# Optimization experiments

Hardware: AMD Instinct MI355X
Metric: run time of the kernel (lower is better)

## Reference

```python
import jax, jax.numpy as jnp
import numpy as np

B, T, M, D, H = 32, 256, 16, 128, 128

def _hard_sigmoid(x):
    # Keras hard_sigmoid: clip(0.2*x + 0.5, 0, 1)
    return jnp.clip(0.2 * x + 0.5, 0.0, 1.0)

def setup_inputs() -> dict:
    key = jax.random.key(0)
    ks = jax.random.split(key, 16)
    s = 0.05  # small init scale, roughly glorot-ish for these dims
    inp = {"x": jax.random.normal(ks[0], (B, T, M, D), jnp.float32)}
    inp["W_a"] = jax.random.normal(ks[1], (D + H, H), jnp.float32) * s
    inp["b_a"] = jnp.zeros((H,), jnp.float32)
    for i, n in enumerate("ifco"):
        inp[f"W_{n}"] = jax.random.normal(ks[2 + 3 * i], (D, H), jnp.float32) * s
        inp[f"U_{n}"] = jax.random.normal(ks[3 + 3 * i], (H, H), jnp.float32) * s
        inp[f"b_{n}"] = jnp.ones((H,), jnp.float32) if n == "f" else jnp.zeros((H,), jnp.float32)
    return inp

def reference(x, W_a, b_a, W_i, U_i, b_i, W_f, U_f, b_f, W_c, U_c, b_c, W_o, U_o, b_o):
    b, t, m, d = x.shape
    h_dim = W_i.shape[1]

    def step(carry, x_t):  # x_t: (B, M, D)
        h, c = carry  # each (B, H)
        hb = jnp.broadcast_to(h[:, None, :], (b, m, h_dim))
        con = jnp.concatenate([x_t, hb], axis=-1)          # (B, M, D+H)
        scores = (con @ W_a + b_a).sum(axis=-1)            # (B, M), linear activation
        sm = jax.nn.softmax(scores, axis=-1)               # (B, M)
        new_x = jnp.einsum('bm,bmd->bd', sm, x_t)          # attention-pooled input
        i_g = _hard_sigmoid(new_x @ W_i + b_i + h @ U_i)
        f_g = _hard_sigmoid(new_x @ W_f + b_f + h @ U_f)
        c_new = f_g * c + i_g * jnp.tanh(new_x @ W_c + b_c + h @ U_c)
        o_g = _hard_sigmoid(new_x @ W_o + b_o + h @ U_o)
        h_new = o_g * jnp.tanh(c_new)
        return (h_new, c_new), None

    h0 = jnp.zeros((b, h_dim), x.dtype)
    c0 = jnp.zeros((b, h_dim), x.dtype)
    (h_last, _), _ = jax.lax.scan(step, (h0, c0), jnp.swapaxes(x, 0, 1))
    return h_last  # return_sequences=False -> last output (B, H)
```

## Files before the change

kernel.cpp:

```cpp
#include <hip/hip_runtime.h>
#include <hip/hip_bf16.h>
#include <hip/hip_fp16.h>

#define BB 32
#define TT 256
#define MM 16
#define DD 128
#define HH 128

typedef unsigned int uint;
typedef unsigned short ushort;

typedef _Float16 f16;
typedef _Float16 f16x8 __attribute__((ext_vector_type(8)));
typedef float f32x4 __attribute__((ext_vector_type(4)));

__device__ __forceinline__ float bl16(uint u){ return __uint_as_float(u << 16); }
__device__ __forceinline__ float bh16(uint u){ return __uint_as_float(u & 0xffff0000u); }

__device__ __forceinline__ float hsig(float x){
  return __builtin_amdgcn_fmed3f(fmaf(x, 0.2f, 0.5f), 0.0f, 1.0f);
}
__device__ __forceinline__ float tanh_f(float x){
  return 1.0f - 2.0f / (__expf(2.0f * x) + 1.0f);
}

__device__ __forceinline__ uint packh2(float a, float b){
  __half2 hv = __floats2half2_rn(a, b);
  union{__half2 h; uint x;} cv; cv.h = hv; return cv.x;
}

__device__ __forceinline__ float qsum4(float v){
  float t1 = __int_as_float(__builtin_amdgcn_mov_dpp(__float_as_int(v), 0xB1, 0xf, 0xf, true));
  v += t1;
  float t2 = __int_as_float(__builtin_amdgcn_mov_dpp(__float_as_int(v), 0x4E, 0xf, 0xf, true));
  return v + t2;
}

__global__ __launch_bounds__(256) void k_prep(
  const void* __restrict__ xraw, const void* __restrict__ Wa,
  const void* __restrict__ U0, const void* __restrict__ U1,
  const void* __restrict__ U2, const void* __restrict__ U3,
  const void* __restrict__ W0, const void* __restrict__ W1,
  const void* __restrict__ W2, const void* __restrict__ W3,
  int* __restrict__ flag, float* __restrict__ vx,
  uint4* __restrict__ Uw, uint4* __restrict__ Ww)
{
  __shared__ int cnt[256];
  __shared__ int smode;
  int tid = threadIdx.x;
  int bid = blockIdx.x;

  {
    const ushort* u = (const ushort*)xraw;
    int c = 0;
    #pragma unroll
    for (int j = 0; j < 8; ++j){
      ushort v = u[2 * (tid * 8 + j)];
      float f = __uint_as_float(((uint)v) << 16);
      if (f == f && fabsf(f) < 64.f && fabsf(f) > 1e-12f) ++c;
    }
    cnt[tid] = c;
    __syncthreads();
    if (tid == 0){
      int s = 0;
      for (int i = 0; i < 256; ++i) s += cnt[i];
      smode = (s > 1024) ? 1 : 0;
    }
    __syncthreads();
  }
  int mode = smode;

  if (bid < 64){
    int idx = (bid & 31) * 256 + tid;
    int f = idx >> 6, lane = idx & 63;
    int g = f >> 5, kc = (f >> 3) & 3, cb = f & 7;
    int k0 = kc * 32 + (lane >> 4) * 8;
    int c  = cb * 16 + (lane & 15);
    const void* Ms[4];
    if (bid < 32){ Ms[0] = U0; Ms[1] = U1; Ms[2] = U2; Ms[3] = U3; }
    else         { Ms[0] = W0; Ms[1] = W1; Ms[2] = W2; Ms[3] = W3; }
    float v[8];
    if (mode){
      const ushort* U = (const ushort*)Ms[g];
      #pragma unroll
      for (int e = 0; e < 8; ++e)
        v[e] = __uint_as_float(((uint)U[(size_t)(k0 + e) * HH + c]) << 16);
    } else {
      const float* U = (const float*)Ms[g];
      #pragma unroll
      for (int e = 0; e < 8; ++e)
        v[e] = U[(size_t)(k0 + e) * HH + c];
    }
    uint4 o;
    o.x = packh2(v[0], v[1]); o.y = packh2(v[2], v[3]);
    o.z = packh2(v[4], v[5]); o.w = packh2(v[6], v[7]);
    ((bid < 32) ? Uw : Ww)[idx] = o;
  } else {
    if (tid == 0) *flag = mode;
    if (tid < 128){
      int d = tid;
      float s = 0.f;
      if (mode){
        const uint4* row = (const uint4*)((const ushort*)Wa + d * HH);
        #pragma unroll
        for (int q = 0; q < 16; ++q){
          uint4 v = row[q];
          s += bl16(v.x) + bh16(v.x) + bl16(v.y) + bh16(v.y)
             + bl16(v.z) + bh16(v.z) + bl16(v.w) + bh16(v.w);
        }
      } else {
        const float4* row = (const float4*)((const float*)Wa + d * HH);
        #pragma unroll
        for (int q = 0; q < 32; ++q){
          float4 v = row[q];
          s += v.x + v.y + v.z + v.w;
        }
      }
      vx[d] = s;
    }
  }
}

__global__ __launch_bounds__(256) void k_pool(const void* __restrict__ xraw,
                                              const int* __restrict__ flag,
                                              const float* __restrict__ vx,
                                              __half* __restrict__ newx){
  __shared__ float xs[2][MM][DD];
  __shared__ float sc[2][MM];
  int mode = *flag;
  int tid = threadIdx.x;
  int half = tid >> 7, t2 = tid & 127;
  int bt = blockIdx.x * 2 + half;
  int b = bt >> 8, t = bt & 255;

  float* xdst = &xs[half][0][0];
  if (mode){
    const float* vxp = vx + (t2 & 15) * 8;
    float4 vra = *(const float4*)vxp;
    float4 vrb = *(const float4*)(vxp + 4);
    const uint4* s = (const uint4*)((const ushort*)xraw + (size_t)bt * 2048);
    float sq[2];
    #pragma unroll
    for (int q = 0; q < 2; ++q){
      int ch = t2 + 128 * q;
      uint4 v = s[ch];
      float* d = &xdst[ch * 8];
      float e0 = bl16(v.x), e1 = bh16(v.x), e2 = bl16(v.y), e3 = bh16(v.y);
      float e4 = bl16(v.z), e5 = bh16(v.z), e6 = bl16(v.w), e7 = bh16(v.w);
      d[0] = e0; d[1] = e1; d[2] = e2; d[3] = e3;
      d[4] = e4; d[5] = e5; d[6] = e6; d[7] = e7;
      float p = e0 * vra.x;
      p = fmaf(e1, vra.y, p); p = fmaf(e2, vra.z, p); p = fmaf(e3, vra.w, p);
      p = fmaf(e4, vrb.x, p); p = fmaf(e5, vrb.y, p); p = fmaf(e6, vrb.z, p);
      p = fmaf(e7, vrb.w, p);
      sq[q] = p;
    }
    #pragma unroll
    for (int q = 0; q < 2; ++q){
      float v = qsum4(sq[q]);
      v += __shfl_xor(v, 4, 16);
      v += __shfl_xor(v, 8, 16);
      sq[q] = v;
    }
    if ((t2 & 15) == 0){
      sc[half][t2 >> 4]       = sq[0];
      sc[half][(t2 >> 4) + 8] = sq[1];
    }
  } else {
    float4 vra = *(const float4*)(vx + (t2 & 31) * 4);
    const float4* s = (const float4*)((const float*)xraw + (size_t)bt * 2048);
    float sq[4];
    #pragma unroll
    for (int q = 0; q < 4; ++q){
      int ch = t2 + 128 * q;
      float4 v = s[ch];
      *(float4*)&xdst[ch * 4] = v;
      float p = v.x * vra.x;
      p = fmaf(v.y, vra.y, p); p = fmaf(v.z, vra.z, p); p = fmaf(v.w, vra.w, p);
      sq[q] = p;
    }
    #pragma unroll
    for (int q = 0; q < 4; ++q){
      float v = qsum4(sq[q]);
      v += __shfl_xor(v, 4, 32);
      v += __shfl_xor(v, 8, 32);
      v += __shfl_xor(v, 16, 32);
      sq[q] = v;
    }
    if ((t2 & 31) == 0){
      int mb = t2 >> 5;
      sc[half][mb]      = sq[0];
      sc[half][mb + 4]  = sq[1];
      sc[half][mb + 8]  = sq[2];
      sc[half][mb + 12] = sq[3];
    }
  }
  __syncthreads();

  float mx = sc[half][0];
  #pragma unroll
  for (int m2 = 1; m2 < MM; ++m2) mx = fmaxf(mx, sc[half][m2]);
  float wgt[MM]; float den = 0.f;
  #pragma unroll
  for (int m2 = 0; m2 < MM; ++m2){ wgt[m2] = __expf(sc[half][m2] - mx); den += wgt[m2]; }
  float inv = 1.0f / den;

  float acc = 0.f;
  #pragma unroll
  for (int m2 = 0; m2 < MM; ++m2)
    acc = fmaf(wgt[m2], xs[half][m2][t2], acc);
  newx[((size_t)t * BB + b) * DD + t2] = __float2half(acc * inv);
}

__global__ __launch_bounds__(256) void k_xproj(const __half* __restrict__ nx,
  const uint4* __restrict__ Ww,
  const void* __restrict__ b0_, const void* __restrict__ b1_,
  const void* __restrict__ b2_, const void* __restrict__ b3_,
  const int* __restrict__ flag, float* __restrict__ Xp)
{
  __shared__ __align__(16) char As[32768];
  int tid = threadIdx.x;
  int r0 = blockIdx.x * 128;
  int G  = blockIdx.y;
  int lane = tid & 63, w = tid >> 6;
  int l16 = lane & 15, lq = lane >> 4;

  {
    const uint4* src = (const uint4*)(nx + (size_t)r0 * DD);
    uint4* dst = (uint4*)As;
    #pragma unroll
    for (int i = 0; i < 8; ++i){
      int gid = i * 256 + tid;
      int r = gid >> 4, c16 = gid & 15;
      dst[r * 16 + (c16 ^ (r & 15))] = src[gid];
    }
  }

  int mode = *flag;
  const void* bb = (G == 0) ? b0_ : (G == 1) ? b1_ : (G == 2) ? b2_ : b3_;
  float bias[8];
  #pragma unroll
  for (int cb = 0; cb < 8; ++cb){
    int col = cb * 16 + l16;
    bias[cb] = mode ? __uint_as_float(((uint)((const ushort*)bb)[col]) << 16)
                    : ((const float*)bb)[col];
  }
  __syncthreads();

  int rb = w * 32;
  f32x4 acc[2][8];
  #pragma unroll
  for (int mt = 0; mt < 2; ++mt)
    #pragma unroll
    for (int cb = 0; cb < 8; ++cb)
      acc[mt][cb] = (f32x4){bias[cb], bias[cb], bias[cb], bias[cb]};

  #pragma unroll
  for (int kc = 0; kc < 4; ++kc){
    f16x8 a[2];
    #pragma unroll
    for (int mt = 0; mt < 2; ++mt){
      int r = rb + mt * 16 + l16;
      int g16 = (kc * 4 + lq) ^ (r & 15);
      a[mt] = *(const f16x8*)(As + r * 256 + g16 * 16);
    }
    #pragma unroll
    for (int cb = 0; cb < 8; ++cb){
      union{uint4 u; f16x8 h;} bv;
      bv.u = Ww[((size_t)((G * 4 + kc) * 8 + cb)) * 64 + lane];
      acc[0][cb] = __builtin_amdgcn_mfma_f32_16x16x32_f16(a[0], bv.h, acc[0][cb], 0, 0, 0);
      acc[1][cb] = __builtin_amdgcn_mfma_f32_16x16x32_f16(a[1], bv.h, acc[1][cb], 0, 0, 0);
    }
  }

  #pragma unroll
  for (int mt = 0; mt < 2; ++mt)
    #pragma unroll
    for (int cb = 0; cb < 8; ++cb)
      #pragma unroll
      for (int reg = 0; reg < 4; ++reg){
        size_t r = (size_t)(r0 + rb + mt * 16 + lq * 4 + reg);
        Xp[r * 512 + G * HH + cb * 16 + l16] = acc[mt][cb][reg];
      }
}

__global__ __attribute__((amdgpu_waves_per_eu(2, 2))) __launch_bounds__(512)
void k_rec(const float* __restrict__ Xp, const uint4* __restrict__ Uw,
           float* __restrict__ out)
{
  __shared__ __align__(16) __half hlds[2][HH];
  int tid  = threadIdx.x;
  int b    = blockIdx.x;
  int w    = tid >> 6;
  int lane = tid & 63;
  int l16  = lane & 15;

  f16x8 Ub[16];
  #pragma unroll
  for (int g = 0; g < 4; ++g)
    #pragma unroll
    for (int kc = 0; kc < 4; ++kc){
      uint4 v = Uw[((g * 4 + kc) * 8 + w) * 64 + lane];
      union{uint4 u; f16x8 h;} cv; cv.u = v;
      Ub[g * 4 + kc] = cv.h;
    }

  const float* xcol = Xp + (size_t)b * 512 + w * 16 + l16;
  float xpA[4], xpB[4];
  #pragma unroll
  for (int g = 0; g < 4; ++g) xpA[g] = xcol[g * 128];
  #pragma unroll
  for (int g = 0; g < 4; ++g) xpB[g] = xcol[(size_t)(BB * 512) + g * 128];

  if (tid < 64) ((uint*)&hlds[0][0])[tid] = 0;
  float cst = 0.f, vh = 0.f;
  const int lo = (lane >> 4) * 16;
  __syncthreads();

#define STEP(T, XP) do{                                                        \
    const char* hb = (const char*)&hlds[(T) & 1][0];                           \
    f16x8 a0 = *(const f16x8*)(hb +   0 + lo);                                 \
    f16x8 a1 = *(const f16x8*)(hb +  64 + lo);                                 \
    f16x8 a2 = *(const f16x8*)(hb + 128 + lo);                                 \
    f16x8 a3 = *(const f16x8*)(hb + 192 + lo);                                 \
    f32x4 c0, c1, c2, c3, d0, d1, d2, d3;                                      \
    c0[0] = XP[0]; c1[0] = XP[1]; c2[0] = XP[2]; c3[0] = XP[3];                \
    d0[0] = 0.f;   d1[0] = 0.f;   d2[0] = 0.f;   d3[0] = 0.f;                  \
    c0 = __builtin_amdgcn_mfma_f32_16x16x32_f16(a0, Ub[ 0], c0, 0, 0, 0);      \
    c1 = __builtin_amdgcn_mfma_f32_16x16x32_f16(a0, Ub[ 4], c1, 0, 0, 0);      \
    c2 = __builtin_amdgcn_mfma_f32_16x16x32_f16(a0, Ub[ 8], c2, 0, 0, 0);      \
    c3 = __builtin_amdgcn_mfma_f32_16x16x32_f16(a0, Ub[12], c3, 0, 0, 0);      \
    d0 = __builtin_amdgcn_mfma_f32_16x16x32_f16(a2, Ub[ 2], d0, 0, 0, 0);      \
    d1 = __builtin_amdgcn_mfma_f32_16x16x32_f16(a2, Ub[ 6], d1, 0, 0, 0);      \
    d2 = __builtin_amdgcn_mfma_f32_16x16x32_f16(a2, Ub[10], d2, 0, 0, 0);      \
    d3 = __builtin_amdgcn_mfma_f32_16x16x32_f16(a2, Ub[14], d3, 0, 0, 0);      \
    c0 = __builtin_amdgcn_mfma_f32_16x16x32_f16(a1, Ub[ 1], c0, 0, 0, 0);      \
    c1 = __builtin_amdgcn_mfma_f32_16x16x32_f16(a1, Ub[ 5], c1, 0, 0, 0);      \
    c2 = __builtin_amdgcn_mfma_f32_16x16x32_f16(a1, Ub[ 9], c2, 0, 0, 0);      \
    c3 = __builtin_amdgcn_mfma_f32_16x16x32_f16(a1, Ub[13], c3, 0, 0, 0);      \
    d0 = __builtin_amdgcn_mfma_f32_16x16x32_f16(a3, Ub[ 3], d0, 0, 0, 0);      \
    d1 = __builtin_amdgcn_mfma_f32_16x16x32_f16(a3, Ub[ 7], d1, 0, 0, 0);      \
    d2 = __builtin_amdgcn_mfma_f32_16x16x32_f16(a3, Ub[11], d2, 0, 0, 0);      \
    d3 = __builtin_amdgcn_mfma_f32_16x16x32_f16(a3, Ub[15], d3, 0, 0, 0);      \
    float p0 = c0[0] + d0[0];                                                  \
    float p1 = c1[0] + d1[0];                                                  \
    float p2 = c2[0] + d2[0];                                                  \
    float p3 = c3[0] + d3[0];                                                  \
    float ig = hsig(p0), fg = hsig(p1), og = hsig(p3);                         \
    float gg = tanh_f(p2);                                                     \
    cst = fmaf(fg, cst, ig * gg);                                              \
    vh  = og * tanh_f(cst);                                                    \
    if (lane < 16) hlds[((T) + 1) & 1][w * 16 + lane] = __float2half(vh);      \
    {                                                                          \
      int tp = (T) + 2; if (tp > TT - 1) tp = TT - 1;                          \
      const float* xs = xcol + ((size_t)tp << 14);                             \
      _Pragma("unroll")                                                        \
      for (int g = 0; g < 4; ++g) XP[g] = xs[g * 128];                         \
    }                                                                          \
    asm volatile("s_waitcnt lgkmcnt(0)" ::: "memory");                         \
    __builtin_amdgcn_s_barrier();                                              \
    asm volatile("" ::: "memory");                                             \
  }while(0)

  for (int t = 0; t < TT; t += 2){
    STEP(t,     xpA);
    STEP(t + 1, xpB);
  }
#undef STEP

  if (lane < 16) out[b * HH + w * 16 + lane] = vh;
}

extern "C" void kernel_launch(void* const* d_in, const int* in_sizes, int n_in,
                              void* d_out, int out_size, void* d_ws, size_t ws_size,
                              hipStream_t stream) {
  (void)in_sizes; (void)n_in; (void)out_size; (void)ws_size;

  char* ws = (char*)d_ws;
  int* flag = (int*)ws;
  float* vx = (float*)(ws + 16);
  uint4* Uw = (uint4*)(ws + 1024);
  uint4* Ww = (uint4*)(ws + 1024 + 131072);
  __half* newx = (__half*)(ws + 1024 + 2 * 131072);
  float* Xp = (float*)(ws + 1024 + 2 * 131072 + (size_t)2 * 1024 * 1024);

  k_prep<<<65, 256, 0, stream>>>(d_in[0], d_in[1],
      d_in[4], d_in[7], d_in[10], d_in[13],
      d_in[3], d_in[6], d_in[9],  d_in[12],
      flag, vx, Uw, Ww);
  k_pool<<<BB * TT / 2, 256, 0, stream>>>(d_in[0], flag, vx, newx);
  dim3 g2(64, 4);
  k_xproj<<<g2, 256, 0, stream>>>(newx, Ww,
      d_in[5], d_in[8], d_in[11], d_in[14],
      flag, Xp);
  k_rec<<<BB, 512, 0, stream>>>(Xp, Uw, (float*)d_out);
}
```

Measured before the change: 251.7 us.

## Fuse prep, pooling, projection and recurrence into one cooperative kernel

Replaces the four separate launches (weight repack, attention pooling, input projection, recurrence) with a single cooperative kernel that separates phases with grid-wide syncs, falling back to the old launches if the cooperative launch fails. This aims to remove launch gaps and kernel-boundary overhead between stages. The trade-off is that the recurrence still runs on only 32 of 256 blocks, the pooling phase is restricted to 256 resident blocks, and grid syncs add their own cost.

Measured after the change: 345.2 us. 37.1% more time.

```diff
diff --git a/kernel.cpp b/kernel.cpp
--- a/kernel.cpp
+++ b/kernel.cpp
@@ -1,12 +1,16 @@
 #include <hip/hip_runtime.h>
+#include <hip/hip_cooperative_groups.h>
 #include <hip/hip_bf16.h>
 #include <hip/hip_fp16.h>
+
+namespace cg = cooperative_groups;
 
 #define BB 32
 #define TT 256
 #define MM 16
 #define DD 128
 #define HH 128
+#define GRID 256
 
 typedef unsigned int uint;
 typedef unsigned short ushort;
@@ -24,17 +28,326 @@
 __device__ __forceinline__ float tanh_f(float x){
   return 1.0f - 2.0f / (__expf(2.0f * x) + 1.0f);
 }
-
 __device__ __forceinline__ uint packh2(float a, float b){
   __half2 hv = __floats2half2_rn(a, b);
   union{__half2 h; uint x;} cv; cv.h = hv; return cv.x;
 }
-
 __device__ __forceinline__ float qsum4(float v){
   float t1 = __int_as_float(__builtin_amdgcn_mov_dpp(__float_as_int(v), 0xB1, 0xf, 0xf, true));
   v += t1;
   float t2 = __int_as_float(__builtin_amdgcn_mov_dpp(__float_as_int(v), 0x4E, 0xf, 0xf, true));
   return v + t2;
+}
+
+__global__ __attribute__((amdgpu_waves_per_eu(2, 2))) __launch_bounds__(512)
+void k_fused(const void* __restrict__ xraw, const void* __restrict__ Wa,
+  const void* __restrict__ U0, const void* __restrict__ U1,
+  const void* __restrict__ U2, const void* __restrict__ U3,
+  const void* __restrict__ W0, const void* __restrict__ W1,
+  const void* __restrict__ W2, const void* __restrict__ W3,
+  const void* __restrict__ b0_, const void* __restrict__ b1_,
+  const void* __restrict__ b2_, const void* __restrict__ b3_,
+  uint4* __restrict__ Uw, uint4* __restrict__ Ww,
+  __half* __restrict__ newx, float* __restrict__ Xp,
+  float* __restrict__ out)
+{
+  __shared__ float xs[4][MM][DD];
+  __shared__ float sc4[4][MM];
+  __shared__ __align__(16) float part4[512];
+  __shared__ __align__(16) float vxs[DD];
+  __shared__ int cnt[256];
+  __shared__ int smode;
+  __shared__ __align__(16) __half hlds[2][HH];
+
+  cg::grid_group grid = cg::this_grid();
+  int tid = threadIdx.x;
+  int bid = blockIdx.x;
+  int lane = tid & 63;
+  int wv = tid >> 6;
+
+  if (tid < 256){
+    const ushort* u = (const ushort*)xraw;
+    int c = 0;
+    #pragma unroll
+    for (int j = 0; j < 8; ++j){
+      ushort v = u[2 * (tid * 8 + j)];
+      float f = __uint_as_float(((uint)v) << 16);
+      if (f == f && fabsf(f) < 64.f && fabsf(f) > 1e-12f) ++c;
+    }
+    cnt[tid] = c;
+  }
+  __syncthreads();
+  if (tid == 0){
+    int s = 0;
+    for (int i = 0; i < 256; ++i) s += cnt[i];
+    smode = (s > 1024) ? 1 : 0;
+  }
+  __syncthreads();
+  int mode = smode;
+
+  {
+    int gtid = bid * 512 + tid;
+    if (gtid < 16384){
+      int half = gtid >> 13;
+      int idx = gtid & 8191;
+      int f = idx >> 6, pl = idx & 63;
+      int g = f >> 5, kc = (f >> 3) & 3, cb = f & 7;
+      int k0 = kc * 32 + (pl >> 4) * 8;
+      int c  = cb * 16 + (pl & 15);
+      const void* Ms[8] = {U0, U1, U2, U3, W0, W1, W2, W3};
+      const void* M = Ms[half * 4 + g];
+      float v[8];
+      if (mode){
+        const ushort* U = (const ushort*)M;
+        #pragma unroll
+        for (int e = 0; e < 8; ++e)
+          v[e] = __uint_as_float(((uint)U[(size_t)(k0 + e) * HH + c]) << 16);
+      } else {
+        const float* U = (const float*)M;
+        #pragma unroll
+        for (int e = 0; e < 8; ++e)
+          v[e] = U[(size_t)(k0 + e) * HH + c];
+      }
+      uint4 o;
+      o.x = packh2(v[0], v[1]); o.y = packh2(v[2], v[3]);
+      o.z = packh2(v[4], v[5]); o.w = packh2(v[6], v[7]);
+      (half ? Ww : Uw)[idx] = o;
+    }
+  }
+
+  {
+    int d = tid >> 2, q = tid & 3;
+    float s = 0.f;
+    if (mode){
+      const uint4* row = (const uint4*)((const ushort*)Wa + d * HH + q * 32);
+      #pragma unroll
+      for (int qq = 0; qq < 4; ++qq){
+        uint4 v = row[qq];
+        s += bl16(v.x) + bh16(v.x) + bl16(v.y) + bh16(v.y)
+           + bl16(v.z) + bh16(v.z) + bl16(v.w) + bh16(v.w);
+      }
+    } else {
+      const float4* row = (const float4*)((const float*)Wa + d * HH + q * 32);
+      #pragma unroll
+      for (int qq = 0; qq < 8; ++qq){
+        float4 v = row[qq];
+        s += v.x + v.y + v.z + v.w;
+      }
+    }
+    part4[tid] = s;
+  }
+  __syncthreads();
+  if (tid < 128)
+    vxs[tid] = part4[4 * tid] + part4[4 * tid + 1] + part4[4 * tid + 2] + part4[4 * tid + 3];
+
+  for (int pass = 0; pass < 8; ++pass){
+    int q4 = tid >> 7, t2 = tid & 127;
+    int bt = pass * 1024 + bid * 4 + q4;
+    int b = bt >> 8, t = bt & 255;
+    float* xdst = &xs[q4][0][0];
+    __syncthreads();
+    if (mode){
+      const float* vxp = &vxs[(t2 & 15) * 8];
+      float4 vra = *(const float4*)vxp;
+      float4 vrb = *(const float4*)(vxp + 4);
+      const uint4* s = (const uint4*)((const ushort*)xraw + (size_t)bt * 2048);
+      float sq[2];
+      #pragma unroll
+      for (int q = 0; q < 2; ++q){
+        int ch = t2 + 128 * q;
+        uint4 v = s[ch];
+        float* d = &xdst[ch * 8];
+        float e0 = bl16(v.x), e1 = bh16(v.x), e2 = bl16(v.y), e3 = bh16(v.y);
+        float e4 = bl16(v.z), e5 = bh16(v.z), e6 = bl16(v.w), e7 = bh16(v.w);
+        d[0] = e0; d[1] = e1; d[2] = e2; d[3] = e3;
+        d[4] = e4; d[5] = e5; d[6] = e6; d[7] = e7;
+        float p = e0 * vra.x;
+        p = fmaf(e1, vra.y, p); p = fmaf(e2, vra.z, p); p = fmaf(e3, vra.w, p);
+        p = fmaf(e4, vrb.x, p); p = fmaf(e5, vrb.y, p); p = fmaf(e6, vrb.z, p);
+        p = fmaf(e7, vrb.w, p);
+        sq[q] = p;
+      }
+      #pragma unroll
+      for (int q = 0; q < 2; ++q){
+        float v = qsum4(sq[q]);
+        v += __shfl_xor(v, 4, 16);
+        v += __shfl_xor(v, 8, 16);
+        sq[q] = v;
+      }
+      if ((t2 & 15) == 0){
+        sc4[q4][t2 >> 4]       = sq[0];
+        sc4[q4][(t2 >> 4) + 8] = sq[1];
+      }
+    } else {
+      float4 vra = *(const float4*)&vxs[(t2 & 31) * 4];
+      const float4* s = (const float4*)((const float*)xraw + (size_t)bt * 2048);
+      float sq[4];
+      #pragma unroll
+      for (int q = 0; q < 4; ++q){
+        int ch = t2 + 128 * q;
+        float4 v = s[ch];
+        *(float4*)&xdst[ch * 4] = v;
+        float p = v.x * vra.x;
+        p = fmaf(v.y, vra.y, p); p = fmaf(v.z, vra.z, p); p = fmaf(v.w, vra.w, p);
+        sq[q] = p;
+      }
+      #pragma unroll
+      for (int q = 0; q < 4; ++q){
+        float v = qsum4(sq[q]);
+        v += __shfl_xor(v, 4, 32);
+        v += __shfl_xor(v, 8, 32);
+        v += __shfl_xor(v, 16, 32);
+        sq[q] = v;
+      }
+      if ((t2 & 31) == 0){
+        int mb = t2 >> 5;
+        sc4[q4][mb]      = sq[0];
+        sc4[q4][mb + 4]  = sq[1];
+        sc4[q4][mb + 8]  = sq[2];
+        sc4[q4][mb + 12] = sq[3];
+      }
+    }
+    __syncthreads();
+
+    float mx = sc4[q4][0];
+    #pragma unroll
+    for (int m2 = 1; m2 < MM; ++m2) mx = fmaxf(mx, sc4[q4][m2]);
+    float wgt[MM]; float den = 0.f;
+    #pragma unroll
+    for (int m2 = 0; m2 < MM; ++m2){ wgt[m2] = __expf(sc4[q4][m2] - mx); den += wgt[m2]; }
+    float inv = 1.0f / den;
+
+    float acc = 0.f;
+    #pragma unroll
+    for (int m2 = 0; m2 < MM; ++m2)
+      acc = fmaf(wgt[m2], xs[q4][m2][t2], acc);
+    newx[((size_t)t * BB + b) * DD + t2] = __float2half(acc * inv);
+  }
+
+  grid.sync();
+
+  {
+    int wg = bid * 8 + wv;
+    int rc = wg >> 2, G = wg & 3;
+    int r0 = rc * 16;
+    int l16 = lane & 15, lq = lane >> 4;
+
+    const void* bb = (G == 0) ? b0_ : (G == 1) ? b1_ : (G == 2) ? b2_ : b3_;
+    float bias[8];
+    #pragma unroll
+    for (int cb = 0; cb < 8; ++cb){
+      int col = cb * 16 + l16;
+      bias[cb] = mode ? __uint_as_float(((uint)((const ushort*)bb)[col]) << 16)
+                      : ((const float*)bb)[col];
+    }
+
+    f16x8 a[4];
+    #pragma unroll
+    for (int kc = 0; kc < 4; ++kc)
+      a[kc] = *(const f16x8*)(newx + (size_t)(r0 + l16) * DD + kc * 32 + lq * 8);
+
+    f32x4 acc[8];
+    #pragma unroll
+    for (int cb = 0; cb < 8; ++cb)
+      acc[cb] = (f32x4){bias[cb], bias[cb], bias[cb], bias[cb]};
+
+    #pragma unroll
+    for (int kc = 0; kc < 4; ++kc)
+      #pragma unroll
+      for (int cb = 0; cb < 8; ++cb){
+        union{uint4 u; f16x8 h;} bv;
+        bv.u = Ww[((size_t)((G * 4 + kc) * 8 + cb)) * 64 + lane];
+        acc[cb] = __builtin_amdgcn_mfma_f32_16x16x32_f16(a[kc], bv.h, acc[cb], 0, 0, 0);
+      }
+
+    #pragma unroll
+    for (int cb = 0; cb < 8; ++cb)
+      #pragma unroll
+      for (int reg = 0; reg < 4; ++reg)
+        Xp[(size_t)(r0 + lq * 4 + reg) * 512 + G * HH + cb * 16 + l16] = acc[cb][reg];
+  }
+
+  grid.sync();
+
+  if (bid < BB){
+    int b = bid;
+    int l16 = lane & 15;
+
+    f16x8 Ub[16];
+    #pragma unroll
+    for (int g = 0; g < 4; ++g)
+      #pragma unroll
+      for (int kc = 0; kc < 4; ++kc){
+        uint4 v = Uw[((g * 4 + kc) * 8 + wv) * 64 + lane];
+        union{uint4 u; f16x8 h;} cv; cv.u = v;
+        Ub[g * 4 + kc] = cv.h;
+      }
+
+    const float* xcol = Xp + (size_t)b * 512 + wv * 16 + l16;
+    float xpA[4], xpB[4];
+    #pragma unroll
+    for (int g = 0; g < 4; ++g) xpA[g] = xcol[g * 128];
+    #pragma unroll
+    for (int g = 0; g < 4; ++g) xpB[g] = xcol[(size_t)(BB * 512) + g * 128];
+
+    if (tid < 64) ((uint*)&hlds[0][0])[tid] = 0;
+    float cst = 0.f, vh = 0.f;
+    const int lo = (lane >> 4) * 16;
+    __syncthreads();
+
+#define STEP(T, XP) do{                                                        \
+    const char* hb = (const char*)&hlds[(T) & 1][0];                           \
+    f16x8 a0 = *(const f16x8*)(hb +   0 + lo);                                 \
+    f16x8 a1 = *(const f16x8*)(hb +  64 + lo);                                 \
+    f16x8 a2 = *(const f16x8*)(hb + 128 + lo);                                 \
+    f16x8 a3 = *(const f16x8*)(hb + 192 + lo);                                 \
+    f32x4 c0, c1, c2, c3, d0, d1, d2, d3;                                      \
+    c0[0] = XP[0]; c1[0] = XP[1]; c2[0] = XP[2]; c3[0] = XP[3];                \
+    d0[0] = 0.f;   d1[0] = 0.f;   d2[0] = 0.f;   d3[0] = 0.f;                  \
+    c0 = __builtin_amdgcn_mfma_f32_16x16x32_f16(a0, Ub[ 0], c0, 0, 0, 0);      \
+    c1 = __builtin_amdgcn_mfma_f32_16x16x32_f16(a0, Ub[ 4], c1, 0, 0, 0);      \
+    c2 = __builtin_amdgcn_mfma_f32_16x16x32_f16(a0, Ub[ 8], c2, 0, 0, 0);      \
+    c3 = __builtin_amdgcn_mfma_f32_16x16x32_f16(a0, Ub[12], c3, 0, 0, 0);      \
+    d0 = __builtin_amdgcn_mfma_f32_16x16x32_f16(a2, Ub[ 2], d0, 0, 0, 0);      \
+    d1 = __builtin_amdgcn_mfma_f32_16x16x32_f16(a2, Ub[ 6], d1, 0, 0, 0);      \
+    d2 = __builtin_amdgcn_mfma_f32_16x16x32_f16(a2, Ub[10], d2, 0, 0, 0);      \
+    d3 = __builtin_amdgcn_mfma_f32_16x16x32_f16(a2, Ub[14], d3, 0, 0, 0);      \
+    c0 = __builtin_amdgcn_mfma_f32_16x16x32_f16(a1, Ub[ 1], c0, 0, 0, 0);      \
+    c1 = __builtin_amdgcn_mfma_f32_16x16x32_f16(a1, Ub[ 5], c1, 0, 0, 0);      \
+    c2 = __builtin_amdgcn_mfma_f32_16x16x32_f16(a1, Ub[ 9], c2, 0, 0, 0);      \
+    c3 = __builtin_amdgcn_mfma_f32_16x16x32_f16(a1, Ub[13], c3, 0, 0, 0);      \
+    d0 = __builtin_amdgcn_mfma_f32_16x16x32_f16(a3, Ub[ 3], d0, 0, 0, 0);      \
+    d1 = __builtin_amdgcn_mfma_f32_16x16x32_f16(a3, Ub[ 7], d1, 0, 0, 0);      \
+    d2 = __builtin_amdgcn_mfma_f32_16x16x32_f16(a3, Ub[11], d2, 0, 0, 0);      \
+    d3 = __builtin_amdgcn_mfma_f32_16x16x32_f16(a3, Ub[15], d3, 0, 0, 0);      \
+    float p0 = c0[0] + d0[0];                                                  \
+    float p1 = c1[0] + d1[0];                                                  \
+    float p2 = c2[0] + d2[0];                                                  \
+    float p3 = c3[0] + d3[0];                                                  \
+    float ig = hsig(p0), fg = hsig(p1), og = hsig(p3);                         \
+    float gg = tanh_f(p2);                                                     \
+    cst = fmaf(fg, cst, ig * gg);                                              \
+    vh  = og * tanh_f(cst);                                                    \
+    if (lane < 16) hlds[((T) + 1) & 1][wv * 16 + lane] = __float2half(vh);     \
+    {                                                                          \
+      int tp = (T) + 2; if (tp > TT - 1) tp = TT - 1;                          \
+      const float* xsrc = xcol + ((size_t)tp << 14);                           \
+      _Pragma("unroll")                                                        \
+      for (int g = 0; g < 4; ++g) XP[g] = xsrc[g * 128];                       \
+    }                                                                          \
+    asm volatile("s_waitcnt lgkmcnt(0)" ::: "memory");                         \
+    __builtin_amdgcn_s_barrier();                                              \
+    asm volatile("" ::: "memory");                                             \
+  }while(0)
+
+    for (int t = 0; t < TT; t += 2){
+      STEP(t,     xpA);
+      STEP(t + 1, xpB);
+    }
+#undef STEP
+
+    if (lane < 16) out[b * HH + wv * 16 + lane] = vh;
+  }
 }
 
 __global__ __launch_bounds__(256) void k_prep(
@@ -50,7 +363,6 @@
   __shared__ int smode;
   int tid = threadIdx.x;
   int bid = blockIdx.x;
-
   {
     const ushort* u = (const ushort*)xraw;
     int c = 0;
@@ -354,9 +666,9 @@
     if (lane < 16) hlds[((T) + 1) & 1][w * 16 + lane] = __float2half(vh);      \
     {                                                                          \
       int tp = (T) + 2; if (tp > TT - 1) tp = TT - 1;                          \
-      const float* xs = xcol + ((size_t)tp << 14);                             \
+      const float* xsrc = xcol + ((size_t)tp << 14);                           \
       _Pragma("unroll")                                                        \
-      for (int g = 0; g < 4; ++g) XP[g] = xs[g * 128];                         \
+      for (int g = 0; g < 4; ++g) XP[g] = xsrc[g * 128];                       \
     }                                                                          \
     asm volatile("s_waitcnt lgkmcnt(0)" ::: "memory");                         \
     __builtin_amdgcn_s_barrier();                                              \
@@ -385,14 +697,37 @@
   __half* newx = (__half*)(ws + 1024 + 2 * 131072);
   float* Xp = (float*)(ws + 1024 + 2 * 131072 + (size_t)2 * 1024 * 1024);
 
-  k_prep<<<65, 256, 0, stream>>>(d_in[0], d_in[1],
-      d_in[4], d_in[7], d_in[10], d_in[13],
-      d_in[3], d_in[6], d_in[9],  d_in[12],
-      flag, vx, Uw, Ww);
-  k_pool<<<BB * TT / 2, 256, 0, stream>>>(d_in[0], flag, vx, newx);
-  dim3 g2(64, 4);
-  k_xproj<<<g2, 256, 0, stream>>>(newx, Ww,
-      d_in[5], d_in[8], d_in[11], d_in[14],
-      flag, Xp);
-  k_rec<<<BB, 512, 0, stream>>>(Xp, Uw, (float*)d_out);
-}
+  void* p_x  = (void*)d_in[0];  void* p_wa = (void*)d_in[1];
+  void* p_u0 = (void*)d_in[4];  void* p_u1 = (void*)d_in[7];
+  void* p_u2 = (void*)d_in[10]; void* p_u3 = (void*)d_in[13];
+  void* p_w0 = (void*)d_in[3];  void* p_w1 = (void*)d_in[6];
+  void* p_w2 = (void*)d_in[9];  void* p_w3 = (void*)d_in[12];
+  void* p_b0 = (void*)d_in[5];  void* p_b1 = (void*)d_in[8];
+  void* p_b2 = (void*)d_in[11]; void* p_b3 = (void*)d_in[14];
+  void* p_out = d_out;
+
+  void* kargs[] = {
+    &p_x, &p_wa,
+    &p_u0, &p_u1, &p_u2, &p_u3,
+    &p_w0, &p_w1, &p_w2, &p_w3,
+    &p_b0, &p_b1, &p_b2, &p_b3,
+    &Uw, &Ww, &newx, &Xp, &p_out
+  };
+
+  hipError_t err = hipLaunchCooperativeKernel(
+      reinterpret_cast<const void*>(&k_fused),
+      dim3(GRID), dim3(512), kargs, 0, stream);
+
+  if (err != hipSuccess){
+    k_prep<<<65, 256, 0, stream>>>(d_in[0], d_in[1],
+        d_in[4], d_in[7], d_in[10], d_in[13],
+        d_in[3], d_in[6], d_in[9],  d_in[12],
+        flag, vx, Uw, Ww);
+    k_pool<<<BB * TT / 2, 256, 0, stream>>>(d_in[0], flag, vx, newx);
+    dim3 g2(64, 4);
+    k_xproj<<<g2, 256, 0, stream>>>(newx, Ww,
+        d_in[5], d_in[8], d_in[11], d_in[14],
+        flag, Xp);
+    k_rec<<<BB, 512, 0, stream>>>(Xp, Uw, (float*)d_out);
+  }
+}
```

## Fuse prep with pooling and fold input projection into recurrent kernel

Applied to the files above, without the earlier changes.

Merges the weight-prep and attention-pooling kernels into one launch: each pooling block recomputes the row sums of W_a in shared memory and redetects the input mode, so no flag or vx buffer is needed. The input-projection GEMM moves into the recurrent kernel, where each batch block computes its own Xp slice before the time loop. This removes two kernel launches and the associated dependencies. In exchange, the projection runs on only 32 blocks with strided loads, which may serialize work that was previously spread across many blocks.

After: 292.8 us. 16.3% more time.

```diff
diff --git a/kernel.cpp b/kernel.cpp
--- a/kernel.cpp
+++ b/kernel.cpp
@@ -24,12 +24,10 @@
 __device__ __forceinline__ float tanh_f(float x){
   return 1.0f - 2.0f / (__expf(2.0f * x) + 1.0f);
 }
-
 __device__ __forceinline__ uint packh2(float a, float b){
   __half2 hv = __floats2half2_rn(a, b);
   union{__half2 h; uint x;} cv; cv.h = hv; return cv.x;
 }
-
 __device__ __forceinline__ float qsum4(float v){
   float t1 = __int_as_float(__builtin_amdgcn_mov_dpp(__float_as_int(v), 0xB1, 0xf, 0xf, true));
   v += t1;
@@ -37,16 +35,20 @@
   return v + t2;
 }
 
-__global__ __launch_bounds__(256) void k_prep(
+
+__global__ __launch_bounds__(256) void k_prep_pool(
   const void* __restrict__ xraw, const void* __restrict__ Wa,
   const void* __restrict__ U0, const void* __restrict__ U1,
   const void* __restrict__ U2, const void* __restrict__ U3,
   const void* __restrict__ W0, const void* __restrict__ W1,
   const void* __restrict__ W2, const void* __restrict__ W3,
-  int* __restrict__ flag, float* __restrict__ vx,
-  uint4* __restrict__ Uw, uint4* __restrict__ Ww)
+  uint4* __restrict__ Uw, uint4* __restrict__ Ww,
+  __half* __restrict__ newx)
 {
-  __shared__ int cnt[256];
+  __shared__ float xs[2][MM][DD];
+  __shared__ float sc[2][MM];
+  __shared__ __align__(16) float vxs[DD];
+  __shared__ int wcnt[4];
   __shared__ int smode;
   int tid = threadIdx.x;
   int bid = blockIdx.x;
@@ -60,13 +62,11 @@
       float f = __uint_as_float(((uint)v) << 16);
       if (f == f && fabsf(f) < 64.f && fabsf(f) > 1e-12f) ++c;
     }
-    cnt[tid] = c;
+    #pragma unroll
+    for (int off = 1; off < 64; off <<= 1) c += __shfl_xor(c, off, 64);
+    if ((tid & 63) == 0) wcnt[tid >> 6] = c;
     __syncthreads();
-    if (tid == 0){
-      int s = 0;
-      for (int i = 0; i < 256; ++i) s += cnt[i];
-      smode = (s > 1024) ? 1 : 0;
-    }
+    if (tid == 0) smode = (wcnt[0] + wcnt[1] + wcnt[2] + wcnt[3] > 1024) ? 1 : 0;
     __syncthreads();
   }
   int mode = smode;
@@ -96,47 +96,40 @@
     o.x = packh2(v[0], v[1]); o.y = packh2(v[2], v[3]);
     o.z = packh2(v[4], v[5]); o.w = packh2(v[6], v[7]);
     ((bid < 32) ? Uw : Ww)[idx] = o;
-  } else {
-    if (tid == 0) *flag = mode;
-    if (tid < 128){
-      int d = tid;
-      float s = 0.f;
-      if (mode){
-        const uint4* row = (const uint4*)((const ushort*)Wa + d * HH);
-        #pragma unroll
-        for (int q = 0; q < 16; ++q){
-          uint4 v = row[q];
-          s += bl16(v.x) + bh16(v.x) + bl16(v.y) + bh16(v.y)
-             + bl16(v.z) + bh16(v.z) + bl16(v.w) + bh16(v.w);
-        }
-      } else {
-        const float4* row = (const float4*)((const float*)Wa + d * HH);
-        #pragma unroll
-        for (int q = 0; q < 32; ++q){
-          float4 v = row[q];
-          s += v.x + v.y + v.z + v.w;
-        }
-      }
-      vx[d] = s;
-    }
-  }
-}
-
-__global__ __launch_bounds__(256) void k_pool(const void* __restrict__ xraw,
-                                              const int* __restrict__ flag,
-                                              const float* __restrict__ vx,
-                                              __half* __restrict__ newx){
-  __shared__ float xs[2][MM][DD];
-  __shared__ float sc[2][MM];
-  int mode = *flag;
-  int tid = threadIdx.x;
+    return;
+  }
+
+  {
+    int d = tid >> 1, q = tid & 1;
+    float s = 0.f;
+    if (mode){
+      const uint4* row = (const uint4*)((const ushort*)Wa + d * HH + q * 64);
+      #pragma unroll
+      for (int qq = 0; qq < 8; ++qq){
+        uint4 v = row[qq];
+        s += bl16(v.x) + bh16(v.x) + bl16(v.y) + bh16(v.y)
+           + bl16(v.z) + bh16(v.z) + bl16(v.w) + bh16(v.w);
+      }
+    } else {
+      const float4* row = (const float4*)((const float*)Wa + d * HH + q * 64);
+      #pragma unroll
+      for (int qq = 0; qq < 16; ++qq){
+        float4 v = row[qq];
+        s += v.x + v.y + v.z + v.w;
+      }
+    }
+    s += __shfl_xor(s, 1, 64);
+    if (q == 0) vxs[d] = s;
+  }
+  __syncthreads();
+
   int half = tid >> 7, t2 = tid & 127;
-  int bt = blockIdx.x * 2 + half;
+  int bt = (bid - 64) * 2 + half;
   int b = bt >> 8, t = bt & 255;
 
   float* xdst = &xs[half][0][0];
   if (mode){
-    const float* vxp = vx + (t2 & 15) * 8;
+    const float* vxp = &vxs[(t2 & 15) * 8];
     float4 vra = *(const float4*)vxp;
     float4 vrb = *(const float4*)(vxp + 4);
     const uint4* s = (const uint4*)((const ushort*)xraw + (size_t)bt * 2048);
@@ -168,7 +161,7 @@
       sc[half][(t2 >> 4) + 8] = sq[1];
     }
   } else {
-    float4 vra = *(const float4*)(vx + (t2 & 31) * 4);
+    float4 vra = *(const float4*)&vxs[(t2 & 31) * 4];
     const float4* s = (const float4*)((const float*)xraw + (size_t)bt * 2048);
     float sq[4];
     #pragma unroll
@@ -213,100 +206,99 @@
   newx[((size_t)t * BB + b) * DD + t2] = __float2half(acc * inv);
 }
 
-__global__ __launch_bounds__(256) void k_xproj(const __half* __restrict__ nx,
-  const uint4* __restrict__ Ww,
-  const void* __restrict__ b0_, const void* __restrict__ b1_,
-  const void* __restrict__ b2_, const void* __restrict__ b3_,
-  const int* __restrict__ flag, float* __restrict__ Xp)
-{
-  __shared__ __align__(16) char As[32768];
-  int tid = threadIdx.x;
-  int r0 = blockIdx.x * 128;
-  int G  = blockIdx.y;
-  int lane = tid & 63, w = tid >> 6;
-  int l16 = lane & 15, lq = lane >> 4;
-
-  {
-    const uint4* src = (const uint4*)(nx + (size_t)r0 * DD);
-    uint4* dst = (uint4*)As;
-    #pragma unroll
-    for (int i = 0; i < 8; ++i){
-      int gid = i * 256 + tid;
-      int r = gid >> 4, c16 = gid & 15;
-      dst[r * 16 + (c16 ^ (r & 15))] = src[gid];
-    }
-  }
-
-  int mode = *flag;
-  const void* bb = (G == 0) ? b0_ : (G == 1) ? b1_ : (G == 2) ? b2_ : b3_;
-  float bias[8];
-  #pragma unroll
-  for (int cb = 0; cb < 8; ++cb){
-    int col = cb * 16 + l16;
-    bias[cb] = mode ? __uint_as_float(((uint)((const ushort*)bb)[col]) << 16)
-                    : ((const float*)bb)[col];
-  }
-  __syncthreads();
-
-  int rb = w * 32;
-  f32x4 acc[2][8];
-  #pragma unroll
-  for (int mt = 0; mt < 2; ++mt)
-    #pragma unroll
-    for (int cb = 0; cb < 8; ++cb)
-      acc[mt][cb] = (f32x4){bias[cb], bias[cb], bias[cb], bias[cb]};
-
-  #pragma unroll
-  for (int kc = 0; kc < 4; ++kc){
-    f16x8 a[2];
-    #pragma unroll
-    for (int mt = 0; mt < 2; ++mt){
-      int r = rb + mt * 16 + l16;
-      int g16 = (kc * 4 + lq) ^ (r & 15);
-      a[mt] = *(const f16x8*)(As + r * 256 + g16 * 16);
-    }
-    #pragma unroll
-    for (int cb = 0; cb < 8; ++cb){
-      union{uint4 u; f16x8 h;} bv;
-      bv.u = Ww[((size_t)((G * 4 + kc) * 8 + cb)) * 64 + lane];
-      acc[0][cb] = __builtin_amdgcn_mfma_f32_16x16x32_f16(a[0], bv.h, acc[0][cb], 0, 0, 0);
-      acc[1][cb] = __builtin_amdgcn_mfma_f32_16x16x32_f16(a[1], bv.h, acc[1][cb], 0, 0, 0);
-    }
-  }
-
-  #pragma unroll
-  for (int mt = 0; mt < 2; ++mt)
-    #pragma unroll
-    for (int cb = 0; cb < 8; ++cb)
-      #pragma unroll
-      for (int reg = 0; reg < 4; ++reg){
-        size_t r = (size_t)(r0 + rb + mt * 16 + lq * 4 + reg);
-        Xp[r * 512 + G * HH + cb * 16 + l16] = acc[mt][cb][reg];
-      }
-}
-
 __global__ __attribute__((amdgpu_waves_per_eu(2, 2))) __launch_bounds__(512)
-void k_rec(const float* __restrict__ Xp, const uint4* __restrict__ Uw,
-           float* __restrict__ out)
+void k_rec2(const void* __restrict__ xraw, const __half* __restrict__ newx,
+            const uint4* __restrict__ Uw, const uint4* __restrict__ Ww,
+            const void* __restrict__ b0_, const void* __restrict__ b1_,
+            const void* __restrict__ b2_, const void* __restrict__ b3_,
+            float* __restrict__ Xp, float* __restrict__ out)
 {
   __shared__ __align__(16) __half hlds[2][HH];
+  __shared__ int wcnt[8];
+  __shared__ int smode;
   int tid  = threadIdx.x;
   int b    = blockIdx.x;
-  int w    = tid >> 6;
+  int wv   = tid >> 6;
   int lane = tid & 63;
-  int l16  = lane & 15;
+  int l16  = lane & 15, lq = lane >> 4;
+
+  {
+    const ushort* u = (const ushort*)xraw;
+    int c = 0;
+    #pragma unroll
+    for (int j = 0; j < 4; ++j){
+      ushort v = u[2 * (tid * 4 + j)];
+      float f = __uint_as_float(((uint)v) << 16);
+      if (f == f && fabsf(f) < 64.f && fabsf(f) > 1e-12f) ++c;
+    }
+    #pragma unroll
+    for (int off = 1; off < 64; off <<= 1) c += __shfl_xor(c, off, 64);
+    if (lane == 0) wcnt[wv] = c;
+    __syncthreads();
+    if (tid == 0){
+      int s = 0;
+      #pragma unroll
+      for (int i = 0; i < 8; ++i) s += wcnt[i];
+      smode = (s > 1024) ? 1 : 0;
+    }
+    __syncthreads();
+  }
+  int mode = smode;
+
+  {
+    int tc0 = wv, tc1 = wv + 8;
+    for (int G = 0; G < 4; ++G){
+      const void* bb = (G == 0) ? b0_ : (G == 1) ? b1_ : (G == 2) ? b2_ : b3_;
+      float bias[8];
+      #pragma unroll
+      for (int cb = 0; cb < 8; ++cb){
+        int col = cb * 16 + l16;
+        bias[cb] = mode ? __uint_as_float(((uint)((const ushort*)bb)[col]) << 16)
+                        : ((const float*)bb)[col];
+      }
+      f32x4 acc0[8], acc1[8];
+      #pragma unroll
+      for (int cb = 0; cb < 8; ++cb){
+        acc0[cb] = (f32x4){bias[cb], bias[cb], bias[cb], bias[cb]};
+        acc1[cb] = (f32x4){bias[cb], bias[cb], bias[cb], bias[cb]};
+      }
+      #pragma unroll
+      for (int kc = 0; kc < 4; ++kc){
+        f16x8 a0 = *(const f16x8*)(newx + ((size_t)(tc0 * 16 + l16) * BB + b) * DD + kc * 32 + lq * 8);
+        f16x8 a1 = *(const f16x8*)(newx + ((size_t)(tc1 * 16 + l16) * BB + b) * DD + kc * 32 + lq * 8);
+        #pragma unroll
+        for (int cb = 0; cb < 8; ++cb){
+          union{uint4 u; f16x8 h;} bv;
+          bv.u = Ww[((size_t)((G * 4 + kc) * 8 + cb)) * 64 + lane];
+          acc0[cb] = __builtin_amdgcn_mfma_f32_16x16x32_f16(a0, bv.h, acc0[cb], 0, 0, 0);
+          acc1[cb] = __builtin_amdgcn_mfma_f32_16x16x32_f16(a1, bv.h, acc1[cb], 0, 0, 0);
+        }
+      }
+      #pragma unroll
+      for (int cb = 0; cb < 8; ++cb)
+        #pragma unroll
+        for (int reg = 0; reg < 4; ++reg){
+          int t0 = tc0 * 16 + lq * 4 + reg;
+          int t1 = tc1 * 16 + lq * 4 + reg;
+          Xp[((size_t)t0 * BB + b) * 512 + G * HH + cb * 16 + l16] = acc0[cb][reg];
+          Xp[((size_t)t1 * BB + b) * 512 + G * HH + cb * 16 + l16] = acc1[cb][reg];
+        }
+    }
+  }
+  asm volatile("s_waitcnt vmcnt(0)" ::: "memory");
+  __syncthreads();
 
   f16x8 Ub[16];
   #pragma unroll
   for (int g = 0; g < 4; ++g)
     #pragma unroll
     for (int kc = 0; kc < 4; ++kc){
-      uint4 v = Uw[((g * 4 + kc) * 8 + w) * 64 + lane];
+      uint4 v = Uw[((g * 4 + kc) * 8 + wv) * 64 + lane];
       union{uint4 u; f16x8 h;} cv; cv.u = v;
       Ub[g * 4 + kc] = cv.h;
     }
 
-  const float* xcol = Xp + (size_t)b * 512 + w * 16 + l16;
+  const float* xcol = Xp + (size_t)b * 512 + wv * 16 + l16;
   float xpA[4], xpB[4];
   #pragma unroll
   for (int g = 0; g < 4; ++g) xpA[g] = xcol[g * 128];
@@ -315,7 +307,7 @@
 
   if (tid < 64) ((uint*)&hlds[0][0])[tid] = 0;
   float cst = 0.f, vh = 0.f;
-  const int lo = (lane >> 4) * 16;
+  const int lo = lq * 16;
   __syncthreads();
 
 #define STEP(T, XP) do{                                                        \
@@ -351,12 +343,12 @@
     float gg = tanh_f(p2);                                                     \
     cst = fmaf(fg, cst, ig * gg);                                              \
     vh  = og * tanh_f(cst);                                                    \
-    if (lane < 16) hlds[((T) + 1) & 1][w * 16 + lane] = __float2half(vh);      \
+    if (lane < 16) hlds[((T) + 1) & 1][wv * 16 + lane] = __float2half(vh);     \
     {                                                                          \
       int tp = (T) + 2; if (tp > TT - 1) tp = TT - 1;                          \
-      const float* xs = xcol + ((size_t)tp << 14);                             \
+      const float* xsrc = xcol + ((size_t)tp << 14);                           \
       _Pragma("unroll")                                                        \
-      for (int g = 0; g < 4; ++g) XP[g] = xs[g * 128];                         \
+      for (int g = 0; g < 4; ++g) XP[g] = xsrc[g * 128];                       \
     }                                                                          \
     asm volatile("s_waitcnt lgkmcnt(0)" ::: "memory");                         \
     __builtin_amdgcn_s_barrier();                                              \
@@ -369,7 +361,7 @@
   }
 #undef STEP
 
-  if (lane < 16) out[b * HH + w * 16 + lane] = vh;
+  if (lane < 16) out[b * HH + wv * 16 + lane] = vh;
 }
 
 extern "C" void kernel_launch(void* const* d_in, const int* in_sizes, int n_in,
@@ -378,21 +370,16 @@
   (void)in_sizes; (void)n_in; (void)out_size; (void)ws_size;
 
   char* ws = (char*)d_ws;
-  int* flag = (int*)ws;
-  float* vx = (float*)(ws + 16);
   uint4* Uw = (uint4*)(ws + 1024);
   uint4* Ww = (uint4*)(ws + 1024 + 131072);
   __half* newx = (__half*)(ws + 1024 + 2 * 131072);
   float* Xp = (float*)(ws + 1024 + 2 * 131072 + (size_t)2 * 1024 * 1024);
 
-  k_prep<<<65, 256, 0, stream>>>(d_in[0], d_in[1],
+  k_prep_pool<<<64 + BB * TT / 2, 256, 0, stream>>>(d_in[0], d_in[1],
       d_in[4], d_in[7], d_in[10], d_in[13],
       d_in[3], d_in[6], d_in[9],  d_in[12],
-      flag, vx, Uw, Ww);
-  k_pool<<<BB * TT / 2, 256, 0, stream>>>(d_in[0], flag, vx, newx);
-  dim3 g2(64, 4);
-  k_xproj<<<g2, 256, 0, stream>>>(newx, Ww,
+      Uw, Ww, newx);
+  k_rec2<<<BB, 512, 0, stream>>>(d_in[0], newx, Uw, Ww,
       d_in[5], d_in[8], d_in[11], d_in[14],
-      flag, Xp);
-  k_rec<<<BB, 512, 0, stream>>>(Xp, Uw, (float*)d_out);
-}
+      Xp, (float*)d_out);
+}
```

## Halve recurrent kernel waves, each wave handling two column blocks

Applied to the files above, without the earlier changes.

The recurrent kernel now runs 4 waves per block instead of 8. Each wave keeps two 16-column slices of the U weights in registers (32 f16x8 fragments) and carries two cell/hidden states. This makes each per-step barrier cover fewer waves and gives each wave more independent MFMA work to interleave. The cost is a doubled per-wave MFMA chain on the serial critical path and higher register pressure, allowed by waves_per_eu set to 1.

Measured after the change: 299.5 us. 19.0% more time.

```diff
diff --git a/kernel.cpp b/kernel.cpp
--- a/kernel.cpp
+++ b/kernel.cpp
@@ -24,18 +24,17 @@
 __device__ __forceinline__ float tanh_f(float x){
   return 1.0f - 2.0f / (__expf(2.0f * x) + 1.0f);
 }
-
 __device__ __forceinline__ uint packh2(float a, float b){
   __half2 hv = __floats2half2_rn(a, b);
   union{__half2 h; uint x;} cv; cv.h = hv; return cv.x;
 }
-
 __device__ __forceinline__ float qsum4(float v){
   float t1 = __int_as_float(__builtin_amdgcn_mov_dpp(__float_as_int(v), 0xB1, 0xf, 0xf, true));
   v += t1;
   float t2 = __int_as_float(__builtin_amdgcn_mov_dpp(__float_as_int(v), 0x4E, 0xf, 0xf, true));
   return v + t2;
 }
+
 
 __global__ __launch_bounds__(256) void k_prep(
   const void* __restrict__ xraw, const void* __restrict__ Wa,
@@ -50,7 +49,6 @@
   __shared__ int smode;
   int tid = threadIdx.x;
   int bid = blockIdx.x;
-
   {
     const ushort* u = (const ushort*)xraw;
     int c = 0;
@@ -285,37 +283,42 @@
       }
 }
 
-__global__ __attribute__((amdgpu_waves_per_eu(2, 2))) __launch_bounds__(512)
+__global__ __attribute__((amdgpu_waves_per_eu(1, 1))) __launch_bounds__(256)
 void k_rec(const float* __restrict__ Xp, const uint4* __restrict__ Uw,
            float* __restrict__ out)
 {
   __shared__ __align__(16) __half hlds[2][HH];
   int tid  = threadIdx.x;
   int b    = blockIdx.x;
-  int w    = tid >> 6;
+  int wv   = tid >> 6;
   int lane = tid & 63;
-  int l16  = lane & 15;
-
-  f16x8 Ub[16];
+  int l16  = lane & 15, lq = lane >> 4;
+
+  f16x8 Ub[2][16];
+  #pragma unroll
+  for (int cb = 0; cb < 2; ++cb)
+    #pragma unroll
+    for (int g = 0; g < 4; ++g)
+      #pragma unroll
+      for (int kc = 0; kc < 4; ++kc){
+        uint4 v = Uw[((g * 4 + kc) * 8 + wv * 2 + cb) * 64 + lane];
+        union{uint4 u; f16x8 h;} cv; cv.u = v;
+        Ub[cb][g * 4 + kc] = cv.h;
+      }
+
+  const float* xcol = Xp + (size_t)b * 512 + wv * 32 + l16;
+  float xpA[8], xpB[8];
   #pragma unroll
   for (int g = 0; g < 4; ++g)
     #pragma unroll
-    for (int kc = 0; kc < 4; ++kc){
-      uint4 v = Uw[((g * 4 + kc) * 8 + w) * 64 + lane];
-      union{uint4 u; f16x8 h;} cv; cv.u = v;
-      Ub[g * 4 + kc] = cv.h;
-    }
-
-  const float* xcol = Xp + (size_t)b * 512 + w * 16 + l16;
-  float xpA[4], xpB[4];
-  #pragma unroll
-  for (int g = 0; g < 4; ++g) xpA[g] = xcol[g * 128];
-  #pragma unroll
-  for (int g = 0; g < 4; ++g) xpB[g] = xcol[(size_t)(BB * 512) + g * 128];
+    for (int cb = 0; cb < 2; ++cb){
+      xpA[g * 2 + cb] = xcol[g * 128 + cb * 16];
+      xpB[g * 2 + cb] = xcol[(size_t)(BB * 512) + g * 128 + cb * 16];
+    }
 
   if (tid < 64) ((uint*)&hlds[0][0])[tid] = 0;
-  float cst = 0.f, vh = 0.f;
-  const int lo = (lane >> 4) * 16;
+  float cst0 = 0.f, cst1 = 0.f, vh0 = 0.f, vh1 = 0.f;
+  const int lo = lq * 16;
   __syncthreads();
 
 #define STEP(T, XP) do{                                                        \
@@ -324,39 +327,60 @@
     f16x8 a1 = *(const f16x8*)(hb +  64 + lo);                                 \
     f16x8 a2 = *(const f16x8*)(hb + 128 + lo);                                 \
     f16x8 a3 = *(const f16x8*)(hb + 192 + lo);                                 \
-    f32x4 c0, c1, c2, c3, d0, d1, d2, d3;                                      \
-    c0[0] = XP[0]; c1[0] = XP[1]; c2[0] = XP[2]; c3[0] = XP[3];                \
-    d0[0] = 0.f;   d1[0] = 0.f;   d2[0] = 0.f;   d3[0] = 0.f;                  \
-    c0 = __builtin_amdgcn_mfma_f32_16x16x32_f16(a0, Ub[ 0], c0, 0, 0, 0);      \
-    c1 = __builtin_amdgcn_mfma_f32_16x16x32_f16(a0, Ub[ 4], c1, 0, 0, 0);      \
-    c2 = __builtin_amdgcn_mfma_f32_16x16x32_f16(a0, Ub[ 8], c2, 0, 0, 0);      \
-    c3 = __builtin_amdgcn_mfma_f32_16x16x32_f16(a0, Ub[12], c3, 0, 0, 0);      \
-    d0 = __builtin_amdgcn_mfma_f32_16x16x32_f16(a2, Ub[ 2], d0, 0, 0, 0);      \
-    d1 = __builtin_amdgcn_mfma_f32_16x16x32_f16(a2, Ub[ 6], d1, 0, 0, 0);      \
-    d2 = __builtin_amdgcn_mfma_f32_16x16x32_f16(a2, Ub[10], d2, 0, 0, 0);      \
-    d3 = __builtin_amdgcn_mfma_f32_16x16x32_f16(a2, Ub[14], d3, 0, 0, 0);      \
-    c0 = __builtin_amdgcn_mfma_f32_16x16x32_f16(a1, Ub[ 1], c0, 0, 0, 0);      \
-    c1 = __builtin_amdgcn_mfma_f32_16x16x32_f16(a1, Ub[ 5], c1, 0, 0, 0);      \
-    c2 = __builtin_amdgcn_mfma_f32_16x16x32_f16(a1, Ub[ 9], c2, 0, 0, 0);      \
-    c3 = __builtin_amdgcn_mfma_f32_16x16x32_f16(a1, Ub[13], c3, 0, 0, 0);      \
-    d0 = __builtin_amdgcn_mfma_f32_16x16x32_f16(a3, Ub[ 3], d0, 0, 0, 0);      \
-    d1 = __builtin_amdgcn_mfma_f32_16x16x32_f16(a3, Ub[ 7], d1, 0, 0, 0);      \
-    d2 = __builtin_amdgcn_mfma_f32_16x16x32_f16(a3, Ub[11], d2, 0, 0, 0);      \
-    d3 = __builtin_amdgcn_mfma_f32_16x16x32_f16(a3, Ub[15], d3, 0, 0, 0);      \
-    float p0 = c0[0] + d0[0];                                                  \
-    float p1 = c1[0] + d1[0];                                                  \
-    float p2 = c2[0] + d2[0];                                                  \
-    float p3 = c3[0] + d3[0];                                                  \
-    float ig = hsig(p0), fg = hsig(p1), og = hsig(p3);                         \
-    float gg = tanh_f(p2);                                                     \
-    cst = fmaf(fg, cst, ig * gg);                                              \
-    vh  = og * tanh_f(cst);                                                    \
-    if (lane < 16) hlds[((T) + 1) & 1][w * 16 + lane] = __float2half(vh);      \
+    f32x4 cc[2][4], dd[2][4];                                                  \
+    _Pragma("unroll")                                                          \
+    for (int cb = 0; cb < 2; ++cb)                                             \
+      _Pragma("unroll")                                                        \
+      for (int g = 0; g < 4; ++g){ cc[cb][g][0] = XP[g * 2 + cb];              \
+                                   dd[cb][g][0] = 0.f; }                       \
+    _Pragma("unroll")                                                          \
+    for (int cb = 0; cb < 2; ++cb)                                             \
+      _Pragma("unroll")                                                        \
+      for (int g = 0; g < 4; ++g){                                             \
+        cc[cb][g] = __builtin_amdgcn_mfma_f32_16x16x32_f16(a0, Ub[cb][g*4+0],  \
+                                                           cc[cb][g], 0,0,0); \
+        dd[cb][g] = __builtin_amdgcn_mfma_f32_16x16x32_f16(a2, Ub[cb][g*4+2],  \
+                                                           dd[cb][g], 0,0,0); \
+      }                                                                        \
+    _Pragma("unroll")                                                          \
+    for (int cb = 0; cb < 2; ++cb)                                             \
+      _Pragma("unroll")                                                        \
+      for (int g = 0; g < 4; ++g){                                             \
+        cc[cb][g] = __builtin_amdgcn_mfma_f32_16x16x32_f16(a1, Ub[cb][g*4+1],  \
+                                                           cc[cb][g], 0,0,0); \
+        dd[cb][g] = __builtin_amdgcn_mfma_f32_16x16x32_f16(a3, Ub[cb][g*4+3],  \
+                                                           dd[cb][g], 0,0,0); \
+      }                                                                        \
+    {                                                                          \
+      float p0 = cc[0][0][0] + dd[0][0][0];                                    \
+      float p1 = cc[0][1][0] + dd[0][1][0];                                    \
+      float p2 = cc[0][2][0] + dd[0][2][0];                                    \
+      float p3 = cc[0][3][0] + dd[0][3][0];                                    \
+      float ig = hsig(p0), fg = hsig(p1), og = hsig(p3);                       \
+      float gg = tanh_f(p2);                                                   \
+      cst0 = fmaf(fg, cst0, ig * gg);                                          \
+      vh0  = og * tanh_f(cst0);                                                \
+      p0 = cc[1][0][0] + dd[1][0][0];                                          \
+      p1 = cc[1][1][0] + dd[1][1][0];                                          \
+      p2 = cc[1][2][0] + dd[1][2][0];                                          \
+      p3 = cc[1][3][0] + dd[1][3][0];                                          \
+      ig = hsig(p0); fg = hsig(p1); og = hsig(p3);                             \
+      gg = tanh_f(p2);                                                         \
+      cst1 = fmaf(fg, cst1, ig * gg);                                          \
+      vh1  = og * tanh_f(cst1);                                                \
+    }                                                                          \
+    if (lane < 16){                                                            \
+      hlds[((T) + 1) & 1][wv * 32 + lane]      = __float2half(vh0);            \
+      hlds[((T) + 1) & 1][wv * 32 + 16 + lane] = __float2half(vh1);            \
+    }                                                                          \
     {                                                                          \
       int tp = (T) + 2; if (tp > TT - 1) tp = TT - 1;                          \
-      const float* xs = xcol + ((size_t)tp << 14);                             \
+      const float* xsrc = xcol + ((size_t)tp << 14);                           \
       _Pragma("unroll")                                                        \
-      for (int g = 0; g < 4; ++g) XP[g] = xs[g * 128];                         \
+      for (int g = 0; g < 4; ++g)                                              \
+        _Pragma("unroll")                                                      \
+        for (int cb = 0; cb < 2; ++cb)                                         \
+          XP[g * 2 + cb] = xsrc[g * 128 + cb * 16];                            \
     }                                                                          \
     asm volatile("s_waitcnt lgkmcnt(0)" ::: "memory");                         \
     __builtin_amdgcn_s_barrier();                                              \
@@ -369,7 +393,10 @@
   }
 #undef STEP
 
-  if (lane < 16) out[b * HH + w * 16 + lane] = vh;
+  if (lane < 16){
+    out[b * HH + wv * 32 + lane]      = vh0;
+    out[b * HH + wv * 32 + 16 + lane] = vh1;
+  }
 }
 
 extern "C" void kernel_launch(void* const* d_in, const int* in_sizes, int n_in,
@@ -394,5 +421,5 @@
   k_xproj<<<g2, 256, 0, stream>>>(newx, Ww,
       d_in[5], d_in[8], d_in[11], d_in[14],
       flag, Xp);
-  k_rec<<<BB, 512, 0, stream>>>(Xp, Uw, (float*)d_out);
-}
+  k_rec<<<BB, 256, 0, stream>>>(Xp, Uw, (float*)d_out);
+}
```
